# Optimization experiments

Measured on AMD Instinct MI355X. Metric: run time of the kernel, lower is better.

The kernel has to match this reference:

```python
import jax, jax.numpy as jnp
import numpy as np

L = 4          # num_layers
H = 512        # hidden_size == input_size
B, S = 8, 4096
LN_EPS = 1e-5


def parallel_scan_log(coeffs, values):
    """h_t = coeffs_t * h_{t-1} + values_t via Hillis-Steele log-step scan.
    coeffs, values: (B, S, H). Faithful to the torch loop incl. clamp."""
    seq_len = coeffs.shape[1]
    a = jnp.clip(coeffs, 1e-08, 1.0 - 1e-08)
    b = values
    num_steps = int(seq_len - 1).bit_length()
    for step in range(num_steps):
        d = 1 << step
        if d >= seq_len:
            break
        a_prev = jnp.pad(a[:, :-d, :], ((0, 0), (d, 0), (0, 0)), constant_values=1.0)
        b_prev = jnp.pad(b[:, :-d, :], ((0, 0), (d, 0), (0, 0)), constant_values=0.0)
        b = a * b_prev + b   # uses old a (matches a_new/b_new then assign)
        a = a * a_prev
    return b


def mingru_layer(x, Wz, bz, Wh, bh):
    # x: (B,S,in) ; Wz,Wh: (H,in) torch Linear layout (y = x @ W.T + b)
    z = jax.nn.sigmoid(jnp.einsum('bsi,hi->bsh', x, Wz) + bz)
    h_tilde = jnp.tanh(jnp.einsum('bsi,hi->bsh', x, Wh) + bh)
    return parallel_scan_log(1.0 - z, z * h_tilde)


def layer_norm(x, g, b):
    mu = jnp.mean(x, axis=-1, keepdims=True)
    var = jnp.mean(jnp.square(x - mu), axis=-1, keepdims=True)
    return (x - mu) * jax.lax.rsqrt(var + LN_EPS) * g + b


def run_layers(x, Wz, bz, Wh, bh, ln_g, ln_b):
    h = x
    for i in range(L):
        h_new = mingru_layer(h, Wz[i], bz[i], Wh[i], bh[i])
        if i > 0:
            h_new = h_new + h  # residual (shapes match for i>0)
        h = layer_norm(h_new, ln_g, ln_b)  # dropout==Identity (p=0)
    return h


def setup_inputs() -> dict:
    key = jax.random.key(0)
    ks = jax.random.split(key, 12)
    lim = 1.0 / np.sqrt(H)  # torch Linear default init range
    u = lambda k, shp: jax.random.uniform(k, shp, jnp.float32, -lim, lim)
    return {
        'x': jax.random.normal(ks[0], (B, S, H), jnp.float32),
        'Wz_f': u(ks[1], (L, H, H)), 'bz_f': u(ks[2], (L, H)),
        'Wh_f': u(ks[3], (L, H, H)), 'bh_f': u(ks[4], (L, H)),
        'Wz_b': u(ks[5], (L, H, H)), 'bz_b': u(ks[6], (L, H)),
        'Wh_b': u(ks[7], (L, H, H)), 'bh_b': u(ks[8], (L, H)),
        'fusion_w': u(ks[9], (H, 2 * H)), 'fusion_b': u(ks[10], (H,)),
        'ln_g': jnp.ones((H,), jnp.float32), 'ln_b': jnp.zeros((H,), jnp.float32),
    }


def reference(x, Wz_f, bz_f, Wh_f, bh_f, Wz_b, bz_b, Wh_b, bh_b, fusion_w, fusion_b, ln_g, ln_b):
    out_fwd = run_layers(x, Wz_f, bz_f, Wh_f, bh_f, ln_g, ln_b)
    x_rev = jnp.flip(x, axis=1)
    out_bwd = jnp.flip(run_layers(x_rev, Wz_b, bz_b, Wh_b, bh_b, ln_g, ln_b), axis=1)
    out_comb = jnp.concatenate([out_fwd, out_bwd], axis=-1)  # (B,S,2H)
    return jnp.einsum('bsk,hk->bsh', out_comb, fusion_w) + fusion_b
```

## Files before the change

kernel.cpp:

```cpp
#include <hip/hip_runtime.h>

#define HID 512
#define SLEN 4096
#define NB 8
#define BSROWS (NB*SLEN)
#define NLAYER 4
#define CHUNKT 128
#define NCHUNK 32

typedef float f32x4 __attribute__((ext_vector_type(4)));
typedef unsigned int u32x4 __attribute__((ext_vector_type(4)));

typedef const __attribute__((address_space(1))) unsigned int* gas_u32p;
typedef __attribute__((address_space(3))) unsigned int* las_u32p;

__device__ __forceinline__ float bf2f(unsigned short u){
  union { unsigned int i; float f; } v; v.i = ((unsigned int)u) << 16; return v.f;
}
__device__ __forceinline__ unsigned short f2bf(float f){
  union { float f; unsigned int i; } v; v.f = f;
  unsigned int u = v.i;
  u = u + 0x7fffu + ((u >> 16) & 1u);
  return (unsigned short)(u >> 16);
}
__device__ __forceinline__ void mfma_bf16(f32x4& acc, u32x4 a, u32x4 b){
  asm("v_mfma_f32_16x16x32_bf16 %0, %1, %2, %0" : "+v"(acc) : "v"(a), "v"(b));
}
__device__ __forceinline__ void mfma_fence(){
  __builtin_amdgcn_sched_barrier(0);
  asm volatile("s_nop 7\n\ts_nop 7\n\ts_nop 7\n\ts_nop 7");
  __builtin_amdgcn_sched_barrier(0);
}
__device__ __forceinline__ void decode_ab(unsigned int v, float& a, float& b){
  a = (float)(v & 0xffffu) * (1.f/65535.f);
  b = fmaf((float)(v >> 16), 2.f/65535.f, -1.f);
}
__device__ __forceinline__ void gload_lds16(const unsigned short* g, unsigned short* l){
  __builtin_amdgcn_global_load_lds((gas_u32p)(const void*)g, (las_u32p)(void*)l, 16, 0, 0);
}
__device__ __forceinline__ int scidx(int row, int col){
  return row*64 + (col ^ (((row>>2)&3)<<4));
}


__global__ __launch_bounds__(256) void prep_w(
    const float* __restrict__ wzf, const float* __restrict__ whf,
    const float* __restrict__ wzb, const float* __restrict__ whb,
    unsigned short* __restrict__ wbf)
{
  int idx = blockIdx.x*256 + threadIdx.x;
  int i8  = idx & 63;
  int o   = (idx >> 6) & 511;
  int m   = (idx >> 15) & 1;
  int l   = (idx >> 16) & 3;
  int dir = idx >> 18;
  const float* src = dir ? (m ? whb : wzb) : (m ? whf : wzf);
  const float* p = src + ((size_t)(l*512 + o)*512 + i8*8);
  float4 v0 = *(const float4*)p;
  float4 v1 = *(const float4*)(p+4);
  unsigned short* q = wbf + ((((size_t)(dir*4 + l)*2 + m)*512 + o)*512 + i8*8);
  u32x4 outv;
  outv[0] = (unsigned)f2bf(v0.x) | ((unsigned)f2bf(v0.y)<<16);
  outv[1] = (unsigned)f2bf(v0.z) | ((unsigned)f2bf(v0.w)<<16);
  outv[2] = (unsigned)f2bf(v1.x) | ((unsigned)f2bf(v1.y)<<16);
  outv[3] = (unsigned)f2bf(v1.z) | ((unsigned)f2bf(v1.w)<<16);
  *(u32x4*)q = outv;
}

__global__ __launch_bounds__(256) void prep_fw(
    const float* __restrict__ fw, unsigned short* __restrict__ outw)
{
  int idx = blockIdx.x*256 + threadIdx.x;
  const float* p = fw + (size_t)idx*8;
  float4 v0 = *(const float4*)p;
  float4 v1 = *(const float4*)(p+4);
  u32x4 outv;
  outv[0] = (unsigned)f2bf(v0.x) | ((unsigned)f2bf(v0.y)<<16);
  outv[1] = (unsigned)f2bf(v0.z) | ((unsigned)f2bf(v0.w)<<16);
  outv[2] = (unsigned)f2bf(v1.x) | ((unsigned)f2bf(v1.y)<<16);
  outv[3] = (unsigned)f2bf(v1.z) | ((unsigned)f2bf(v1.w)<<16);
  *(u32x4*)(outw + (size_t)idx*8) = outv;
}

__global__ __launch_bounds__(256) void prep_x(
    const float* __restrict__ x, unsigned short* __restrict__ X0)
{
  int idx = blockIdx.x*256 + threadIdx.x;
  int j8  = idx & 63;
  int s   = (idx >> 6) & 4095;
  int b   = (idx >> 18) & 7;
  int dir = idx >> 21;
  int srcs = dir ? (4095 - s) : s;
  const float* p = x + ((size_t)(b*SLEN + srcs)*512 + j8*8);
  float4 v0 = *(const float4*)p;
  float4 v1 = *(const float4*)(p+4);
  u32x4 outv;
  outv[0] = (unsigned)f2bf(v0.x) | ((unsigned)f2bf(v0.y)<<16);
  outv[1] = (unsigned)f2bf(v0.z) | ((unsigned)f2bf(v0.w)<<16);
  outv[2] = (unsigned)f2bf(v1.x) | ((unsigned)f2bf(v1.y)<<16);
  outv[3] = (unsigned)f2bf(v1.z) | ((unsigned)f2bf(v1.w)<<16);
  *(u32x4*)(X0 + ((size_t)((dir*NB + b)*SLEN + s)*512 + j8*8)) = outv;
}


__global__ __launch_bounds__(256) void gate_gemm_scan(
    const unsigned short* __restrict__ X,
    const unsigned short* __restrict__ Wz,
    const unsigned short* __restrict__ Wh,
    const float* __restrict__ bzp, const float* __restrict__ bhp,
    unsigned int* __restrict__ PH,
    float* __restrict__ Aagg, float* __restrict__ Bagg,
    int Mtiles, int CG)
{
  __shared__ __align__(16) unsigned char smem[32768 + 2048];
  unsigned short* As  = (unsigned short*)smem;
  unsigned short* Bzs = (unsigned short*)(smem + 16384);
  unsigned short* Bhs = (unsigned short*)(smem + 24576);
  unsigned int*   SC  = (unsigned int*)smem;
  float* SegP = (float*)(smem + 32768);
  float* SegH = (float*)(smem + 32768 + 1024);

  int hw = blockIdx.x;
  int lg = (hw & 7)*Mtiles + (hw >> 3);
  int nt  = lg & 7;
  int mt  = lg >> 3;

  const int tid = threadIdx.x;
  const int lane = tid & 63;
  const int wv = tid >> 6;
  const int n0 = nt*64;
  const int lrow  = lane >> 3;
  const int slotp = (lane & 7) ^ (lrow & 7);

  f32x4 accz[2][4], acch[2][4];
  #pragma unroll
  for (int i=0;i<2;++i)
    #pragma unroll
    for (int j=0;j<4;++j){ accz[i][j] = (f32x4)(0.f); acch[i][j] = (f32x4)(0.f); }

  for (int ks=0; ks<8; ++ks){
    int k0 = ks*64;
    #pragma unroll
    for (int it=0; it<4; ++it){
      int row = it*32 + wv*8 + lrow;
      gload_lds16(X + (size_t)(mt*128 + row)*512 + k0 + slotp*8,
                  As + (it*32 + wv*8)*64);
    }
    #pragma unroll
    for (int it=0; it<2; ++it){
      int row = it*32 + wv*8 + lrow;
      gload_lds16(Wz + (size_t)(n0 + row)*512 + k0 + slotp*8,
                  Bzs + (it*32 + wv*8)*64);
      gload_lds16(Wh + (size_t)(n0 + row)*512 + k0 + slotp*8,
                  Bhs + (it*32 + wv*8)*64);
    }
    __syncthreads();
    #pragma unroll
    for (int kk=0; kk<2; ++kk){
      int kslot = kk*4 + (lane >> 4);
      u32x4 af[2];
      #pragma unroll
      for (int mf=0; mf<2; ++mf){
        int row = wv*32 + mf*16 + (lane & 15);
        af[mf] = *(const u32x4*)(As + row*64 + ((kslot ^ (row&7))<<3));
      }
      #pragma unroll
      for (int nf=0; nf<4; ++nf){
        int row = nf*16 + (lane & 15);
        u32x4 bz = *(const u32x4*)(Bzs + row*64 + ((kslot ^ (row&7))<<3));
        u32x4 bh = *(const u32x4*)(Bhs + row*64 + ((kslot ^ (row&7))<<3));
        #pragma unroll
        for (int mf=0; mf<2; ++mf){
          mfma_bf16(accz[mf][nf], af[mf], bz);
          mfma_bf16(acch[mf][nf], af[mf], bh);
        }
      }
    }
    __syncthreads();
  }
  mfma_fence();

  #pragma unroll
  for (int nf=0; nf<4; ++nf){
    int colL = nf*16 + (lane & 15);
    float bz = bzp[n0 + colL];
    float bh = bhp[n0 + colL];
    #pragma unroll
    for (int mf=0; mf<2; ++mf){
      int rloc = wv*32 + mf*16 + ((lane>>4)<<2);
      #pragma unroll
      for (int r=0; r<4; ++r){
        float zp = accz[mf][nf][r] + bz;
        float hp = acch[mf][nf][r] + bh;
        float sg = 1.f/(1.f + __expf(-zp));
        float th = 1.f - 2.f/(1.f + __expf(2.f*hp));
        float a = 1.f - sg;
        a = fminf(fmaxf(a, 1e-8f), 1.0f);
        float bv = sg*th;
        unsigned aq = (unsigned)fmaf(a, 65535.f, 0.5f);
        unsigned bq = (unsigned)fmaf(bv, 32767.5f, 32768.0f);
        SC[scidx(rloc + r, colL)] = aq | (bq << 16);
      }
    }
  }
  __syncthreads();

  const int col = tid & 63;
  const int seg = tid >> 6;
  float P = 1.f, Hl = 0.f;
  #pragma unroll
  for (int r=0; r<32; ++r){
    int row = seg*32 + r;
    float a, b; decode_ab(SC[scidx(row, col)], a, b);
    Hl = fmaf(a, Hl, b);
    P *= a;
    unsigned pq = (unsigned)fmaf(P, 65535.f, 0.5f);
    SC[scidx(row, col)] = pq | ((unsigned)f2bf(Hl) << 16);
  }
  SegP[seg*64 + col] = P;
  SegH[seg*64 + col] = Hl;
  __syncthreads();

  float Ppre = 1.f, Hpre = 0.f;
  for (int j=0; j<seg; ++j){
    Hpre = fmaf(SegP[j*64 + col], Hpre, SegH[j*64 + col]);
    Ppre *= SegP[j*64 + col];
  }

  const int rowbase = mt*128;
  float Pg = 1.f, Hg = 0.f;
  #pragma unroll
  for (int r=0; r<32; ++r){
    int row = seg*32 + r;
    unsigned v = SC[scidx(row, col)];
    float Pl = (float)(v & 0xffffu) * (1.f/65535.f);
    float Hlv = bf2f((unsigned short)(v >> 16));
    Pg = Ppre * Pl;
    Hg = fmaf(Pl, Hpre, Hlv);
    unsigned pq = (unsigned)fmaf(Pg, 65535.f, 0.5f);
    PH[(size_t)(rowbase + row)*512 + n0 + col] = pq | ((unsigned)f2bf(Hg) << 16);
  }
  if (seg == 3){
    int chain = (mt >> 5)*512 + n0 + col;
    int c = mt & 31;
    Aagg[c*CG + chain] = Pg;
    Bagg[c*CG + chain] = Hg;
  }
}


__global__ __launch_bounds__(256) void scan_p2(
    const float* __restrict__ Aagg, const float* __restrict__ Bagg,
    float* __restrict__ Hin, int CG)
{
  int chain = blockIdx.x*256 + threadIdx.x;
  float hv = 0.f;
  #pragma unroll
  for (int c=0; c<NCHUNK; ++c){
    Hin[c*CG + chain] = hv;
    hv = fmaf(Aagg[c*CG + chain], hv, Bagg[c*CG + chain]);
  }
}


__global__ __launch_bounds__(256) void recon_ln(
    const unsigned int* __restrict__ PH,
    const float* __restrict__ Hin,
    unsigned short* __restrict__ Xio,
    const float* __restrict__ g, const float* __restrict__ bta,
    int resid, int CG)
{
  int token = blockIdx.x*4 + (threadIdx.x >> 6);
  int lane = threadIdx.x & 63;
  size_t base = (size_t)token*512 + lane*8;
  u32x4 p0 = *(const u32x4*)(PH + base);
  u32x4 p1 = *(const u32x4*)(PH + base + 4);
  int c  = (token >> 7) & 31;
  int bl = token >> 12;
  const float* hin = Hin + (size_t)c*CG + bl*512 + lane*8;
  f32x4 h0 = *(const f32x4*)hin;
  f32x4 h1 = *(const f32x4*)(hin + 4);
  float v[8];
  #pragma unroll
  for (int j=0; j<4; ++j){
    v[j]   = fmaf((float)(p0[j] & 0xffffu)*(1.f/65535.f), h0[j], bf2f((unsigned short)(p0[j] >> 16)));
    v[4+j] = fmaf((float)(p1[j] & 0xffffu)*(1.f/65535.f), h1[j], bf2f((unsigned short)(p1[j] >> 16)));
  }
  if (resid){
    u32x4 xv = *(const u32x4*)(Xio + base);
    #pragma unroll
    for (int w=0; w<4; ++w){
      v[2*w]   += bf2f((unsigned short)(xv[w] & 0xffffu));
      v[2*w+1] += bf2f((unsigned short)(xv[w] >> 16));
    }
  }
  float s = 0.f, s2 = 0.f;
  #pragma unroll
  for (int j=0; j<8; ++j){ s += v[j]; s2 += v[j]*v[j]; }
  #pragma unroll
  for (int o=1; o<64; o<<=1){ s += __shfl_xor(s, o, 64); s2 += __shfl_xor(s2, o, 64); }
  float mu = s * (1.f/512.f);
  float var = s2 * (1.f/512.f) - mu*mu;
  float inv = rsqrtf(var + 1e-5f);
  float4 g0 = *(const float4*)(g + lane*8);
  float4 g1 = *(const float4*)(g + lane*8 + 4);
  float4 b0 = *(const float4*)(bta + lane*8);
  float4 b1 = *(const float4*)(bta + lane*8 + 4);
  float gg[8]  = {g0.x,g0.y,g0.z,g0.w,g1.x,g1.y,g1.z,g1.w};
  float bbv[8] = {b0.x,b0.y,b0.z,b0.w,b1.x,b1.y,b1.z,b1.w};
  u32x4 outv;
  #pragma unroll
  for (int w=0; w<4; ++w){
    float y0 = (v[2*w]   - mu)*inv*gg[2*w]   + bbv[2*w];
    float y1 = (v[2*w+1] - mu)*inv*gg[2*w+1] + bbv[2*w+1];
    outv[w] = (unsigned)f2bf(y0) | ((unsigned)f2bf(y1) << 16);
  }
  *(u32x4*)(Xio + base) = outv;
}


__global__ __launch_bounds__(256) void fusion_gemm(
    const unsigned short* __restrict__ Xf,
    const unsigned short* __restrict__ Wf,
    const float* __restrict__ fb,
    float* __restrict__ outp)
{
  __shared__ __align__(16) unsigned short As[128*64];
  __shared__ __align__(16) unsigned short Bs[64*64];

  int hw = blockIdx.x;
  int lg = (hw & 7)*256 + (hw >> 3);
  int nt = lg & 7;
  int mt = lg >> 3;

  const int tid = threadIdx.x;
  const int lane = tid & 63;
  const int wv = tid >> 6;
  const int n0 = nt*64;
  const int lrow  = lane >> 3;
  const int slotp = (lane & 7) ^ (lrow & 7);

  f32x4 acc[2][4];
  #pragma unroll
  for (int i=0;i<2;++i)
    #pragma unroll
    for (int j=0;j<4;++j) acc[i][j] = (f32x4)(0.f);

  for (int ks=0; ks<16; ++ks){
    int k0 = ks*64;
    const unsigned short* Abase = Xf + ((k0 >= 512) ? (size_t)BSROWS*512 : 0);
    int kc = k0 & 511;
    int flip = (k0 >= 512) ? 4095 : 0;
    #pragma unroll
    for (int it=0; it<4; ++it){
      int row = it*32 + wv*8 + lrow;
      int sr = (mt*128 + row) ^ flip;
      gload_lds16(Abase + (size_t)sr*512 + kc + slotp*8,
                  As + (it*32 + wv*8)*64);
    }
    #pragma unroll
    for (int it=0; it<2; ++it){
      int row = it*32 + wv*8 + lrow;
      gload_lds16(Wf + (size_t)(n0 + row)*1024 + k0 + slotp*8,
                  Bs + (it*32 + wv*8)*64);
    }
    __syncthreads();
    #pragma unroll
    for (int kk=0; kk<2; ++kk){
      int kslot = kk*4 + (lane >> 4);
      u32x4 af[2];
      #pragma unroll
      for (int mf=0; mf<2; ++mf){
        int row = wv*32 + mf*16 + (lane & 15);
        af[mf] = *(const u32x4*)(As + row*64 + ((kslot ^ (row&7))<<3));
      }
      #pragma unroll
      for (int nf=0; nf<4; ++nf){
        int row = nf*16 + (lane & 15);
        u32x4 bv = *(const u32x4*)(Bs + row*64 + ((kslot ^ (row&7))<<3));
        #pragma unroll
        for (int mf=0; mf<2; ++mf) mfma_bf16(acc[mf][nf], af[mf], bv);
      }
    }
    __syncthreads();
  }
  mfma_fence();

  #pragma unroll
  for (int nf=0; nf<4; ++nf){
    int col = n0 + nf*16 + (lane & 15);
    float bias = fb[col];
    #pragma unroll
    for (int mf=0; mf<2; ++mf){
      int rb = mt*128 + wv*32 + mf*16 + ((lane>>4)<<2);
      #pragma unroll
      for (int r=0; r<4; ++r)
        outp[(size_t)(rb + r)*512 + col] = acc[mf][nf][r] + bias;
    }
  }
}


extern "C" void kernel_launch(void* const* d_in, const int* in_sizes, int n_in,
                              void* d_out, int out_size, void* d_ws, size_t ws_size,
                              hipStream_t stream)
{
  (void)in_sizes; (void)n_in; (void)out_size;
  const float* x   = (const float*)d_in[0];
  const float* wzf = (const float*)d_in[1];
  const float* bzf = (const float*)d_in[2];
  const float* whf = (const float*)d_in[3];
  const float* bhf = (const float*)d_in[4];
  const float* wzb = (const float*)d_in[5];
  const float* bzb = (const float*)d_in[6];
  const float* whb = (const float*)d_in[7];
  const float* bhb = (const float*)d_in[8];
  const float* fw  = (const float*)d_in[9];
  const float* fbb = (const float*)d_in[10];
  const float* lng = (const float*)d_in[11];
  const float* lnb = (const float*)d_in[12];
  float* outp = (float*)d_out;

  const size_t WbfB = (size_t)16*512*512*2;
  const size_t WfbB = (size_t)512*1024*2;
  const size_t XB   = (size_t)2*BSROWS*512*2;
  const size_t aggB = (size_t)4096*NCHUNK*4;
  int SG = 8;
  for (int c = 1; c <= 8; c <<= 1){
    size_t need = WbfB + WfbB + XB + 3*aggB
                + ((size_t)BSROWS/c)*512*4
                + 1024;
    if (need <= ws_size){ SG = c; break; }
  }
  const int R  = BSROWS / SG;
  const int NBg = NB / SG;
  const int CG = NBg * 512;
  const int Mtiles = R / 128;

  char* ws = (char*)d_ws;
  size_t o = 0;
  unsigned short* Wbf = (unsigned short*)(ws + o); o += WbfB;
  unsigned short* Wfb = (unsigned short*)(ws + o); o += WfbB;
  unsigned short* X   = (unsigned short*)(ws + o); o += XB;
  unsigned int*   PH  = (unsigned int*)  (ws + o); o += (size_t)R*512*4;
  float* Aagg = (float*)(ws + o); o += aggB;
  float* Bagg = (float*)(ws + o); o += aggB;
  float* Hin  = (float*)(ws + o); o += aggB;

  prep_w <<<2048, 256, 0, stream>>>(wzf, whf, wzb, whb, Wbf);
  prep_fw<<<256,  256, 0, stream>>>(fw, Wfb);
  prep_x <<<16384,256, 0, stream>>>(x, X);

  for (int dir = 0; dir < 2; ++dir){
    const float* bz = dir ? bzb : bzf;
    const float* bh = dir ? bhb : bhf;
    for (int g = 0; g < SG; ++g){
      unsigned short* Xg = X + ((size_t)dir*BSROWS + (size_t)g*R)*512;
      for (int l = 0; l < NLAYER; ++l){
        const unsigned short* Wz = Wbf + ((size_t)((dir*4 + l)*2 + 0))*(512*512);
        const unsigned short* Wh = Wbf + ((size_t)((dir*4 + l)*2 + 1))*(512*512);
        gate_gemm_scan<<<Mtiles*8, 256, 0, stream>>>(Xg, Wz, Wh, bz + l*512, bh + l*512,
                                                     PH, Aagg, Bagg, Mtiles, CG);
        scan_p2 <<<CG/256, 256, 0, stream>>>(Aagg, Bagg, Hin, CG);
        recon_ln<<<R/4,    256, 0, stream>>>(PH, Hin, Xg, lng, lnb, l > 0 ? 1 : 0, CG);
      }
    }
  }
  fusion_gemm<<<2048, 256, 0, stream>>>(X, Wfb, fbb, outp);
}
```

Before: 736.3 us.

## Read reversed input via row flip in GEMM load instead of materialized reversed copy

prep_x now writes only the forward bf16 copy of x. The backward direction's first layer reads it with a row-index XOR flip inside gate_gemm_scan, which halves the prep_x traffic. Because of that, the A/B tile loads move from direct global-to-LDS loads to register loads followed by swizzled LDS stores. The in-block scan also drops its write-back of local prefixes to shared memory and recomputes them in the second pass. The register-staged loads may cost more than the async LDS path, which could offset the savings.

```diff
diff --git a/kernel.cpp b/kernel.cpp
--- a/kernel.cpp
+++ b/kernel.cpp
@@ -88,10 +88,8 @@
   int idx = blockIdx.x*256 + threadIdx.x;
   int j8  = idx & 63;
   int s   = (idx >> 6) & 4095;
-  int b   = (idx >> 18) & 7;
-  int dir = idx >> 21;
-  int srcs = dir ? (4095 - s) : s;
-  const float* p = x + ((size_t)(b*SLEN + srcs)*512 + j8*8);
+  int b   = idx >> 18;
+  const float* p = x + ((size_t)(b*SLEN + s)*512 + j8*8);
   float4 v0 = *(const float4*)p;
   float4 v1 = *(const float4*)(p+4);
   u32x4 outv;
@@ -99,7 +97,7 @@
   outv[1] = (unsigned)f2bf(v0.z) | ((unsigned)f2bf(v0.w)<<16);
   outv[2] = (unsigned)f2bf(v1.x) | ((unsigned)f2bf(v1.y)<<16);
   outv[3] = (unsigned)f2bf(v1.z) | ((unsigned)f2bf(v1.w)<<16);
-  *(u32x4*)(X0 + ((size_t)((dir*NB + b)*SLEN + s)*512 + j8*8)) = outv;
+  *(u32x4*)(X0 + ((size_t)(b*SLEN + s)*512 + j8*8)) = outv;
 }
 
 
@@ -110,7 +108,7 @@
     const float* __restrict__ bzp, const float* __restrict__ bhp,
     unsigned int* __restrict__ PH,
     float* __restrict__ Aagg, float* __restrict__ Bagg,
-    int Mtiles, int CG)
+    int Mtiles, int CG, int flip)
 {
   __shared__ __align__(16) unsigned char smem[32768 + 2048];
   unsigned short* As  = (unsigned short*)smem;
@@ -129,8 +127,8 @@
   const int lane = tid & 63;
   const int wv = tid >> 6;
   const int n0 = nt*64;
-  const int lrow  = lane >> 3;
-  const int slotp = (lane & 7) ^ (lrow & 7);
+  const int slot = tid & 7;
+  const int rowb = tid >> 3;
 
   f32x4 accz[2][4], acch[2][4];
   #pragma unroll
@@ -142,17 +140,18 @@
     int k0 = ks*64;
     #pragma unroll
     for (int it=0; it<4; ++it){
-      int row = it*32 + wv*8 + lrow;
-      gload_lds16(X + (size_t)(mt*128 + row)*512 + k0 + slotp*8,
-                  As + (it*32 + wv*8)*64);
+      int row = rowb + it*32;
+      int sr = (mt*128 + row) ^ flip;
+      u32x4 v = *(const u32x4*)(X + (size_t)sr*512 + k0 + slot*8);
+      *(u32x4*)(As + row*64 + ((slot ^ (row&7))<<3)) = v;
     }
     #pragma unroll
     for (int it=0; it<2; ++it){
-      int row = it*32 + wv*8 + lrow;
-      gload_lds16(Wz + (size_t)(n0 + row)*512 + k0 + slotp*8,
-                  Bzs + (it*32 + wv*8)*64);
-      gload_lds16(Wh + (size_t)(n0 + row)*512 + k0 + slotp*8,
-                  Bhs + (it*32 + wv*8)*64);
+      int row = rowb + it*32;
+      u32x4 vz = *(const u32x4*)(Wz + (size_t)(n0+row)*512 + k0 + slot*8);
+      *(u32x4*)(Bzs + row*64 + ((slot ^ (row&7))<<3)) = vz;
+      u32x4 vh = *(const u32x4*)(Wh + (size_t)(n0+row)*512 + k0 + slot*8);
+      *(u32x4*)(Bhs + row*64 + ((slot ^ (row&7))<<3)) = vh;
     }
     __syncthreads();
     #pragma unroll
@@ -207,18 +206,17 @@
 
   const int col = tid & 63;
   const int seg = tid >> 6;
-  float P = 1.f, Hl = 0.f;
-  #pragma unroll
-  for (int r=0; r<32; ++r){
-    int row = seg*32 + r;
-    float a, b; decode_ab(SC[scidx(row, col)], a, b);
-    Hl = fmaf(a, Hl, b);
-    P *= a;
-    unsigned pq = (unsigned)fmaf(P, 65535.f, 0.5f);
-    SC[scidx(row, col)] = pq | ((unsigned)f2bf(Hl) << 16);
-  }
-  SegP[seg*64 + col] = P;
-  SegH[seg*64 + col] = Hl;
+  {
+    float P = 1.f, Hl = 0.f;
+    #pragma unroll 8
+    for (int r=0; r<32; ++r){
+      float a, b; decode_ab(SC[scidx(seg*32 + r, col)], a, b);
+      Hl = fmaf(a, Hl, b);
+      P *= a;
+    }
+    SegP[seg*64 + col] = P;
+    SegH[seg*64 + col] = Hl;
+  }
   __syncthreads();
 
   float Ppre = 1.f, Hpre = 0.f;
@@ -228,15 +226,16 @@
   }
 
   const int rowbase = mt*128;
+  float pl = 1.f, hl = 0.f;
   float Pg = 1.f, Hg = 0.f;
-  #pragma unroll
+  #pragma unroll 8
   for (int r=0; r<32; ++r){
     int row = seg*32 + r;
-    unsigned v = SC[scidx(row, col)];
-    float Pl = (float)(v & 0xffffu) * (1.f/65535.f);
-    float Hlv = bf2f((unsigned short)(v >> 16));
-    Pg = Ppre * Pl;
-    Hg = fmaf(Pl, Hpre, Hlv);
+    float a, b; decode_ab(SC[scidx(row, col)], a, b);
+    hl = fmaf(a, hl, b);
+    pl *= a;
+    Pg = Ppre * pl;
+    Hg = fmaf(pl, Hpre, hl);
     unsigned pq = (unsigned)fmaf(Pg, 65535.f, 0.5f);
     PH[(size_t)(rowbase + row)*512 + n0 + col] = pq | ((unsigned)f2bf(Hg) << 16);
   }
@@ -449,22 +448,40 @@
 
   prep_w <<<2048, 256, 0, stream>>>(wzf, whf, wzb, whb, Wbf);
   prep_fw<<<256,  256, 0, stream>>>(fw, Wfb);
-  prep_x <<<16384,256, 0, stream>>>(x, X);
-
-  for (int dir = 0; dir < 2; ++dir){
-    const float* bz = dir ? bzb : bzf;
-    const float* bh = dir ? bhb : bhf;
-    for (int g = 0; g < SG; ++g){
-      unsigned short* Xg = X + ((size_t)dir*BSROWS + (size_t)g*R)*512;
-      for (int l = 0; l < NLAYER; ++l){
-        const unsigned short* Wz = Wbf + ((size_t)((dir*4 + l)*2 + 0))*(512*512);
-        const unsigned short* Wh = Wbf + ((size_t)((dir*4 + l)*2 + 1))*(512*512);
-        gate_gemm_scan<<<Mtiles*8, 256, 0, stream>>>(Xg, Wz, Wh, bz + l*512, bh + l*512,
-                                                     PH, Aagg, Bagg, Mtiles, CG);
-        scan_p2 <<<CG/256, 256, 0, stream>>>(Aagg, Bagg, Hin, CG);
-        recon_ln<<<R/4,    256, 0, stream>>>(PH, Hin, Xg, lng, lnb, l > 0 ? 1 : 0, CG);
-      }
-    }
-  }
+  prep_x <<<8192, 256, 0, stream>>>(x, X);
+
+  #define CHAIN(Xin_, Xg_, WzP_, WhP_, bzP_, bhP_, flip_, resid_)            \
+    do {                                                                     \
+      gate_gemm_scan<<<Mtiles*8, 256, 0, stream>>>(Xin_, WzP_, WhP_,         \
+          bzP_, bhP_, PH, Aagg, Bagg, Mtiles, CG, flip_);                    \
+      scan_p2 <<<CG/256, 256, 0, stream>>>(Aagg, Bagg, Hin, CG);             \
+      recon_ln<<<R/4,    256, 0, stream>>>(PH, Hin, Xg_, lng, lnb, resid_, CG); \
+    } while (0)
+
+  for (int g = 0; g < SG; ++g){
+    unsigned short* X0g = X + (size_t)g*R*512;
+    unsigned short* X1g = X + ((size_t)BSROWS + (size_t)g*R)*512;
+    const unsigned short* Wz = Wbf + ((size_t)((1*4 + 0)*2 + 0))*(512*512);
+    const unsigned short* Wh = Wbf + ((size_t)((1*4 + 0)*2 + 1))*(512*512);
+    CHAIN(X0g, X1g, Wz, Wh, bzb + 0*512, bhb + 0*512, 4095, 0);
+  }
+  for (int g = 0; g < SG; ++g){
+    unsigned short* X0g = X + (size_t)g*R*512;
+    for (int l = 0; l < NLAYER; ++l){
+      const unsigned short* Wz = Wbf + ((size_t)((0*4 + l)*2 + 0))*(512*512);
+      const unsigned short* Wh = Wbf + ((size_t)((0*4 + l)*2 + 1))*(512*512);
+      CHAIN(X0g, X0g, Wz, Wh, bzf + l*512, bhf + l*512, 0, l > 0 ? 1 : 0);
+    }
+  }
+  for (int g = 0; g < SG; ++g){
+    unsigned short* X1g = X + ((size_t)BSROWS + (size_t)g*R)*512;
+    for (int l = 1; l < NLAYER; ++l){
+      const unsigned short* Wz = Wbf + ((size_t)((1*4 + l)*2 + 0))*(512*512);
+      const unsigned short* Wh = Wbf + ((size_t)((1*4 + l)*2 + 1))*(512*512);
+      CHAIN(X1g, X1g, Wz, Wh, bzb + l*512, bhb + l*512, 0, 1);
+    }
+  }
+  #undef CHAIN
+
   fusion_gemm<<<2048, 256, 0, stream>>>(X, Wfb, fbb, outp);
 }
```

Result: faster. 700.8 us (-4.8%).
